# Performance work log

Hardware: AMD Instinct MI355X
Metric: run time of the kernel (lower is better)

Reference implementation:

```python
import jax, jax.numpy as jnp
import numpy as np

HIDDEN = 1024
NUM_HEADS = 16
HEAD_DIM = HIDDEN // NUM_HEADS


def setup_inputs() -> dict:
    key = jax.random.key(0)
    k1, k2, k3, k4, k5 = jax.random.split(key, 5)
    B, S, T, H = 2, 2048, 2048, HIDDEN
    scale = 0.02
    return {
        "query": jax.random.normal(k1, (B, S, H), dtype=jnp.float32),
        "key_value": jax.random.normal(k2, (B, T, H), dtype=jnp.float32),
        "Wq": jax.random.normal(k3, (H, H), dtype=jnp.float32) * scale,
        "Wkv": jax.random.normal(k4, (H, 2 * H), dtype=jnp.float32) * scale,
        "Wc": jax.random.normal(k5, (H, H), dtype=jnp.float32) * scale,
    }


def reference(query, key_value, Wq, Wkv, Wc):
    B, S, H = query.shape
    T = key_value.shape[1]
    nh, hd = NUM_HEADS, HEAD_DIM

    q = query @ Wq                                  # [B,S,H]
    kv = key_value @ Wkv                            # [B,T,2H]
    k, v = kv[..., :H], kv[..., H:]

    # [B, nh, S|T, hd]
    q = q.reshape(B, S, nh, hd).transpose(0, 2, 1, 3)
    k = k.reshape(B, T, nh, hd).transpose(0, 2, 1, 3)
    v = v.reshape(B, T, nh, hd).transpose(0, 2, 1, 3)

    scale = hd ** -0.5
    scores = jnp.einsum("bhsd,bhtd->bhst", q * scale, k)   # [B,nh,S,T]
    probs = jax.nn.softmax(scores, axis=-1)
    y = jnp.einsum("bhst,bhtd->bhsd", probs, v)             # [B,nh,S,hd]
    y = y.transpose(0, 2, 1, 3).reshape(B, S, H)
    return y @ Wc
```

## Files before the change

kernel.cpp:

```cpp
#include <hip/hip_runtime.h>
#include <hip/hip_bf16.h>


typedef unsigned short u16;
typedef __attribute__((ext_vector_type(4))) float float4v;
typedef __attribute__((ext_vector_type(4))) unsigned short u16x4;
typedef __attribute__((ext_vector_type(8))) short short8;
typedef __attribute__((ext_vector_type(4))) float floatx4;

__device__ __forceinline__ u16 f2bf(float f) {
  unsigned u = __float_as_uint(f);
  u += 0x7fffu + ((u >> 16) & 1u);
  return (u16)(u >> 16);
}

__device__ __forceinline__ float fast_exp2(float x) {
#if __has_builtin(__builtin_amdgcn_exp2f)
  return __builtin_amdgcn_exp2f(x);
#else
  return exp2f(x);
#endif
}

__device__ __forceinline__ unsigned pack_bf2(float a, float b) {
#if __has_builtin(__builtin_amdgcn_cvt_pk_bf16_f32)
  auto r = __builtin_amdgcn_cvt_pk_bf16_f32(a, b);
  unsigned u;
  __builtin_memcpy(&u, &r, 4);
  return u;
#else
  unsigned ua = __float_as_uint(a) + 0x7fffu + ((__float_as_uint(a) >> 16) & 1u);
  unsigned ub = __float_as_uint(b) + 0x7fffu + ((__float_as_uint(b) >> 16) & 1u);
  return __builtin_amdgcn_perm(ub, ua, 0x07060302u);
#endif
}

__device__ __forceinline__ void gld16(const void* g, void* l) {
  __builtin_amdgcn_global_load_lds(
      (const __attribute__((address_space(1))) void*)g,
      (__attribute__((address_space(3))) void*)l, 16, 0, 0);
}

__device__ __forceinline__ int swz4(int r) { return (r & 3) ^ ((r >> 2) & 3); }

__global__ void prep(const float* __restrict__ X, const float* __restrict__ KV,
                     const float* __restrict__ Wq, const float* __restrict__ Wkv,
                     const float* __restrict__ Wc,
                     u16* __restrict__ qin, u16* __restrict__ kvin,
                     u16* __restrict__ Wqt, u16* __restrict__ Wkvt,
                     u16* __restrict__ Wct) {
  __shared__ float tile[32][33];
  const int bid = blockIdx.x, t = threadIdx.x;
  if (bid < 8192) {
    const float* src = bid < 4096 ? X : KV;
    u16* dst = bid < 4096 ? qin : kvin;
    int i = (bid & 4095) * 256 + t;
    float4v v = ((const float4v*)src)[i];
    u16x4 o;
    o.x = f2bf(v.x); o.y = f2bf(v.y); o.z = f2bf(v.z); o.w = f2bf(v.w);
    ((u16x4*)dst)[i] = o;
  } else {
    int r = bid - 8192;
    const float* in;
    u16* out;
    int C, bx, by;
    if (r < 1024)      { in = Wq;  out = Wqt;  C = 1024; bx = r & 31; by = r >> 5; }
    else if (r < 3072) { r -= 1024; in = Wkv; out = Wkvt; C = 2048; bx = r & 63; by = r >> 6; }
    else               { r -= 3072; in = Wc;  out = Wct;  C = 1024; bx = r & 31; by = r >> 5; }
    const int tx = t & 31, ty = t >> 5;
#pragma unroll
    for (int i = 0; i < 32; i += 8)
      tile[ty + i][tx] = in[(size_t)(by * 32 + ty + i) * C + bx * 32 + tx];
    __syncthreads();
#pragma unroll
    for (int i = 0; i < 32; i += 8)
      out[(size_t)(bx * 32 + ty + i) * 1024 + by * 32 + tx] = f2bf(tile[tx][ty + i]);
  }
}

__global__ __launch_bounds__(256, 3) void gemm_qkv(const u16* __restrict__ qin,
                                                   const u16* __restrict__ kvin,
                                                   const u16* __restrict__ Wqt,
                                                   const u16* __restrict__ Wkvt,
                                                   u16* __restrict__ qp,
                                                   u16* __restrict__ kp,
                                                   u16* __restrict__ vt,
                                                   float qscale) {
  __shared__ __align__(16) u16 As[2 * 4096];
  __shared__ __align__(16) u16 Bs[2 * 4096];
  const int t = threadIdx.x;
  const int w = t >> 6, l = t & 63;
  const int lane15 = l & 15, quad = l >> 4;
  const int wm = w >> 1, wn = w & 1;
  const int bm = blockIdx.y * 128;

  const int bx = blockIdx.x;
  const int mode = bx >> 3;
  const u16* A = (mode == 0) ? qin : kvin;
  const u16* Bt = (mode == 0) ? Wqt : Wkvt;
  const int bn = (mode == 2) ? 1024 + (bx - 16) * 128 : (bx & 7) * 128;

  const int srow = t >> 2;
  const int scol = (((t & 3) ^ swz4(srow)) << 3);
  const u16* ag0 = A + (size_t)(bm + srow) * 1024 + scol;
  const u16* ag1 = ag0 + (size_t)64 * 1024;
  const u16* bg0 = Bt + (size_t)(bn + srow) * 1024 + scol;
  const u16* bg1 = bg0 + (size_t)64 * 1024;

  int afo[4], bfo[4];
#pragma unroll
  for (int mi = 0; mi < 4; ++mi) {
    int row = wm * 64 + mi * 16 + lane15;
    afo[mi] = row * 32 + ((quad ^ swz4(row)) << 3);
  }
#pragma unroll
  for (int ni = 0; ni < 4; ++ni) {
    int row = wn * 64 + ni * 16 + lane15;
    bfo[ni] = row * 32 + ((quad ^ swz4(row)) << 3);
  }

  floatx4 acc[4][4] = {};
  const bool vswap = (mode == 2);

  auto stage = [&](int kt, int buf) {
    gld16(ag0 + kt, &As[buf * 4096 + t * 8]);
    gld16(ag1 + kt, &As[buf * 4096 + 2048 + t * 8]);
    gld16(bg0 + kt, &Bs[buf * 4096 + t * 8]);
    gld16(bg1 + kt, &Bs[buf * 4096 + 2048 + t * 8]);
  };
  auto compute = [&](int buf) {
    short8 af[4], bf[4];
#pragma unroll
    for (int mi = 0; mi < 4; ++mi) af[mi] = *(const short8*)&As[buf * 4096 + afo[mi]];
#pragma unroll
    for (int ni = 0; ni < 4; ++ni) bf[ni] = *(const short8*)&Bs[buf * 4096 + bfo[ni]];
    if (!vswap) {
#pragma unroll
      for (int mi = 0; mi < 4; ++mi)
#pragma unroll
        for (int ni = 0; ni < 4; ++ni)
          acc[mi][ni] = __builtin_amdgcn_mfma_f32_16x16x32_bf16(af[mi], bf[ni],
                                                                acc[mi][ni], 0, 0, 0);
    } else {
#pragma unroll
      for (int mi = 0; mi < 4; ++mi)
#pragma unroll
        for (int ni = 0; ni < 4; ++ni)
          acc[mi][ni] = __builtin_amdgcn_mfma_f32_16x16x32_bf16(bf[ni], af[mi],
                                                                acc[mi][ni], 0, 0, 0);
    }
  };

  stage(0, 0);
  __syncthreads();
  for (int kt = 0; kt < 1024; kt += 64) {
    if (kt + 32 < 1024) stage(kt + 32, 1);
    compute(0);
    __syncthreads();
    if (kt + 64 < 1024) stage(kt + 64, 0);
    compute(1);
    __syncthreads();
  }

  if (mode == 0) {
#pragma unroll
    for (int mi = 0; mi < 4; ++mi)
#pragma unroll
      for (int ni = 0; ni < 4; ++ni) {
        int col = bn + wn * 64 + ni * 16 + lane15;
#pragma unroll
        for (int r = 0; r < 4; ++r) {
          int row = bm + wm * 64 + mi * 16 + quad * 4 + r;
          qp[(size_t)row * 1024 + col] = f2bf(acc[mi][ni][r] * qscale);
        }
      }
  } else if (mode == 1) {
#pragma unroll
    for (int mi = 0; mi < 4; ++mi)
#pragma unroll
      for (int ni = 0; ni < 4; ++ni) {
        int col = bn + wn * 64 + ni * 16 + lane15;
#pragma unroll
        for (int r = 0; r < 4; ++r) {
          int row = bm + wm * 64 + mi * 16 + quad * 4 + r;
          kp[(size_t)row * 1024 + col] = f2bf(acc[mi][ni][r]);
        }
      }
  } else {
    const int b = bm >> 11;
    const int tbase = (bm & 2047) + wm * 64;
#pragma unroll
    for (int mi = 0; mi < 4; ++mi)
#pragma unroll
      for (int ni = 0; ni < 4; ++ni) {
        int tloc = tbase + mi * 16 + lane15;
#pragma unroll
        for (int r = 0; r < 4; ++r) {
          int wc = (bn - 1024) + wn * 64 + ni * 16 + quad * 4 + r;
          vt[(size_t)(b * 1024 + wc) * 2048 + tloc] = f2bf(acc[mi][ni][r]);
        }
      }
  }
}

template <typename OutT, int NI>
__device__ __forceinline__ void gemm_body(const u16* __restrict__ A,
                                          const u16* __restrict__ Bt,
                                          OutT* __restrict__ C,
                                          int N, int lda, int Klen, float scale,
                                          int bm, int bn,
                                          u16* As, u16* Bs) {
  const int t = threadIdx.x;
  const int w = t >> 6, l = t & 63;
  const int lane15 = l & 15, quad = l >> 4;
  const int wm = w >> 1, wn = w & 1;
  const int BSZ = NI * 1024;

  const int srow = t >> 2;
  const int scol = (((t & 3) ^ swz4(srow)) << 3);
  const u16* ag0 = A + (size_t)(bm + srow) * lda + scol;
  const u16* ag1 = ag0 + (size_t)64 * lda;
  const u16* bg0 = Bt + (size_t)(bn + srow) * lda + scol;
  const u16* bg1 = bg0 + (size_t)64 * lda;

  int afo[4], bfo[NI];
#pragma unroll
  for (int mi = 0; mi < 4; ++mi) {
    int row = wm * 64 + mi * 16 + lane15;
    afo[mi] = row * 32 + ((quad ^ swz4(row)) << 3);
  }
#pragma unroll
  for (int ni = 0; ni < NI; ++ni) {
    int row = wn * (NI * 16) + ni * 16 + lane15;
    bfo[ni] = row * 32 + ((quad ^ swz4(row)) << 3);
  }

  floatx4 acc[4][NI] = {};

  auto stage = [&](int kt, int ab, int bb) {
    gld16(ag0 + kt, &As[ab + t * 8]);
    gld16(ag1 + kt, &As[ab + 2048 + t * 8]);
    gld16(bg0 + kt, &Bs[bb + t * 8]);
    if (NI == 4) gld16(bg1 + kt, &Bs[bb + 2048 + t * 8]);
  };
  auto compute = [&](int ab, int bb) {
    short8 af[4], bf[NI];
#pragma unroll
    for (int mi = 0; mi < 4; ++mi) af[mi] = *(const short8*)&As[ab + afo[mi]];
#pragma unroll
    for (int ni = 0; ni < NI; ++ni) bf[ni] = *(const short8*)&Bs[bb + bfo[ni]];
#pragma unroll
    for (int mi = 0; mi < 4; ++mi)
#pragma unroll
      for (int ni = 0; ni < NI; ++ni)
        acc[mi][ni] = __builtin_amdgcn_mfma_f32_16x16x32_bf16(af[mi], bf[ni],
                                                              acc[mi][ni], 0, 0, 0);
  };

  stage(0, 0, 0);
  __syncthreads();
  for (int kt = 0; kt < Klen; kt += 64) {
    if (kt + 32 < Klen) stage(kt + 32, 4096, BSZ);
    compute(0, 0);
    __syncthreads();
    if (kt + 64 < Klen) stage(kt + 64, 0, 0);
    compute(4096, BSZ);
    __syncthreads();
  }

#pragma unroll
  for (int mi = 0; mi < 4; ++mi)
#pragma unroll
    for (int ni = 0; ni < NI; ++ni) {
      int col = bn + wn * (NI * 16) + ni * 16 + lane15;
#pragma unroll
      for (int r = 0; r < 4; ++r) {
        int row = bm + wm * 64 + mi * 16 + quad * 4 + r;
        if constexpr (sizeof(OutT) == 4)
          C[(size_t)row * N + col] = acc[mi][ni][r] * scale;
        else
          C[(size_t)row * N + col] = f2bf(acc[mi][ni][r] * scale);
      }
    }
}

__global__ __launch_bounds__(256, 4) void gemm_out(const u16* __restrict__ A,
                                                   const u16* __restrict__ Bt,
                                                   float* __restrict__ C) {
  __shared__ __align__(16) u16 As[2 * 4096];
  __shared__ __align__(16) u16 Bs[2 * 2048];
  gemm_body<float, 2>(A, Bt, C, 1024, 1024, 1024, 1.0f, blockIdx.y * 128,
                      blockIdx.x * 64, As, Bs);
}

__global__ __launch_bounds__(512) void attn_kern(const u16* __restrict__ Q,
                                                 const u16* __restrict__ KP,
                                                 const u16* __restrict__ VT,
                                                 u16* __restrict__ Y) {
  __shared__ __align__(16) u16 Ks[2 * 4096];
  __shared__ __align__(16) u16 VTs[2 * 4096];
  __shared__ __align__(16) u16 Ps[8192];
  const int t = threadIdx.x, w = t >> 6, l = t & 63;
  const int lane15 = l & 15, quad = l >> 4;
  const int bh = blockIdx.y, b = bh >> 4, h = bh & 15;
  const int qrow0 = b * 2048 + blockIdx.x * 128;
  const int xm = lane15 & 7;

  short8 qf[2];
#pragma unroll
  for (int ks = 0; ks < 2; ++ks)
    qf[ks] = *(const short8*)&Q[(size_t)(qrow0 + w * 16 + lane15) * 1024 +
                                h * 64 + ks * 32 + quad * 8];

  const short8 vones = {0x3F80, 0x3F80, 0x3F80, 0x3F80,
                        0x3F80, 0x3F80, 0x3F80, 0x3F80};

  floatx4 yacc[4] = {};
  floatx4 lacc = {};

  const int srow = t >> 3;
  const int scol = (((t & 7) ^ (srow & 7)) << 3);
  const u16* kg = KP + (size_t)(b * 2048 + srow) * 1024 + h * 64 + scol;
  const u16* vg = VT + (size_t)(bh * 64 + srow) * 2048 + scol;

  const int prow = (w * 16 + lane15) * 64;
  int kfo[2][4], vfo[2][4], pwo[4], pro[2];
#pragma unroll
  for (int ks = 0; ks < 2; ++ks)
#pragma unroll
    for (int ti = 0; ti < 4; ++ti)
      kfo[ks][ti] = (ti * 16 + lane15) * 64 + (((ks * 4 + quad) ^ xm) << 3);
#pragma unroll
  for (int ts = 0; ts < 2; ++ts) {
#pragma unroll
    for (int ni = 0; ni < 4; ++ni)
      vfo[ts][ni] = (ni * 16 + lane15) * 64 + (((ts * 4 + quad) ^ xm) << 3);
    pro[ts] = prow + (((ts * 4 + quad) ^ xm) << 3);
  }
#pragma unroll
  for (int ti = 0; ti < 4; ++ti)
    pwo[ti] = prow + (((ti * 2 + (quad >> 1)) ^ xm) << 3) + ((quad & 1) << 2);

  auto stage = [&](int t0n, int buf) {
    gld16(kg + (size_t)t0n * 1024, &Ks[buf + t * 8]);
    gld16(vg + t0n, &VTs[buf + t * 8]);
  };
  auto compute = [&](int buf) {
    floatx4 sacc[4] = {};
#pragma unroll
    for (int ks = 0; ks < 2; ++ks)
#pragma unroll
      for (int ti = 0; ti < 4; ++ti) {
        short8 kf = *(const short8*)&Ks[buf + kfo[ks][ti]];
        sacc[ti] = __builtin_amdgcn_mfma_f32_16x16x32_bf16(kf, qf[ks], sacc[ti], 0, 0, 0);
      }
#pragma unroll
    for (int ti = 0; ti < 4; ++ti) {
      float p0 = fast_exp2(sacc[ti][0]);
      float p1 = fast_exp2(sacc[ti][1]);
      float p2 = fast_exp2(sacc[ti][2]);
      float p3 = fast_exp2(sacc[ti][3]);
      uint2 pk;
      pk.x = pack_bf2(p0, p1);
      pk.y = pack_bf2(p2, p3);
      *(uint2*)&Ps[pwo[ti]] = pk;
    }
#pragma unroll
    for (int ts = 0; ts < 2; ++ts) {
      short8 pf = *(const short8*)&Ps[pro[ts]];
      lacc = __builtin_amdgcn_mfma_f32_16x16x32_bf16(pf, vones, lacc, 0, 0, 0);
#pragma unroll
      for (int ni = 0; ni < 4; ++ni) {
        short8 vf = *(const short8*)&VTs[buf + vfo[ts][ni]];
        yacc[ni] = __builtin_amdgcn_mfma_f32_16x16x32_bf16(pf, vf, yacc[ni], 0, 0, 0);
      }
    }
  };

  stage(0, 0);
  __syncthreads();
  for (int t0 = 0; t0 < 2048; t0 += 128) {
    if (t0 + 64 < 2048) stage(t0 + 64, 4096);
    compute(0);
    __syncthreads();
    if (t0 + 128 < 2048) stage(t0 + 128, 0);
    compute(4096);
    __syncthreads();
  }

#pragma unroll
  for (int r = 0; r < 4; ++r) {
    float linv = 1.0f / lacc[r];
    int row = qrow0 + w * 16 + quad * 4 + r;
#pragma unroll
    for (int ni = 0; ni < 4; ++ni)
      Y[(size_t)row * 1024 + h * 64 + ni * 16 + lane15] = f2bf(yacc[ni][r] * linv);
  }
}

extern "C" void kernel_launch(void* const* d_in, const int* in_sizes, int n_in,
                              void* d_out, int out_size, void* d_ws, size_t ws_size,
                              hipStream_t stream) {
  const float* query = (const float*)d_in[0];
  const float* key_value = (const float*)d_in[1];
  const float* Wq = (const float*)d_in[2];
  const float* Wkv = (const float*)d_in[3];
  const float* Wc = (const float*)d_in[4];
  float* out = (float*)d_out;

  const size_t MB = 1024 * 1024;
  char* ws = (char*)d_ws;
  u16* qin  = (u16*)(ws + 0 * MB);
  u16* kvin = (u16*)(ws + 8 * MB);
  u16* Wqt  = (u16*)(ws + 16 * MB);
  u16* Wkvt = (u16*)(ws + 18 * MB);
  u16* Wct  = (u16*)(ws + 22 * MB);
  u16* qp   = (u16*)(ws + 24 * MB);
  u16* kp   = (u16*)(ws + 32 * MB);
  u16* vt   = (u16*)(ws + 40 * MB);
  u16* y    = (u16*)(ws + 48 * MB);

  prep<<<dim3(12288), dim3(256), 0, stream>>>(query, key_value, Wq, Wkv, Wc,
                                              qin, kvin, Wqt, Wkvt, Wct);
  const float qscale = 0.125f * 1.4426950408889634f;
  gemm_qkv<<<dim3(24, 32), dim3(256), 0, stream>>>(qin, kvin, Wqt, Wkvt,
                                                   qp, kp, vt, qscale);
  attn_kern<<<dim3(16, 32), dim3(512), 0, stream>>>(qp, kp, vt, y);
  gemm_out<<<dim3(16, 32), dim3(256), 0, stream>>>(y, Wct, out);
}
```

Before: 224.7 us.

## Stage GEMM epilogues through LDS and remap blocks for XCD locality

GEMM epilogues now write accumulators into swizzled shared memory and then emit 16-byte coalesced global stores, including the transposed V output that previously used scattered 2-byte stores. All three kernels switch to a 1D grid with a block-index remap that groups neighbouring tiles onto the same XCD to improve L2 reuse. This adds an extra LDS round trip and barriers in the epilogue.

```diff
diff --git a/kernel.cpp b/kernel.cpp
--- a/kernel.cpp
+++ b/kernel.cpp
@@ -86,15 +86,20 @@
                                                    u16* __restrict__ kp,
                                                    u16* __restrict__ vt,
                                                    float qscale) {
-  __shared__ __align__(16) u16 As[2 * 4096];
-  __shared__ __align__(16) u16 Bs[2 * 4096];
+  __shared__ __align__(16) u16 Shm[16384];
+  u16* As = Shm;
+  u16* Bs = Shm + 8192;
   const int t = threadIdx.x;
   const int w = t >> 6, l = t & 63;
   const int lane15 = l & 15, quad = l >> 4;
   const int wm = w >> 1, wn = w & 1;
-  const int bm = blockIdx.y * 128;
-
-  const int bx = blockIdx.x;
+
+  const int bid = blockIdx.x;
+  const int xr = bid & 7, g = bid >> 3;
+  const int bx = 12 * (xr & 1) + g % 12;
+  const int by = 8 * (xr >> 1) + g / 12;
+  const int bm = by * 128;
+
   const int mode = bx >> 3;
   const u16* A = (mode == 0) ? qin : kvin;
   const u16* Bt = (mode == 0) ? Wqt : Wkvt;
@@ -162,135 +167,129 @@
     __syncthreads();
   }
 
-  if (mode == 0) {
-#pragma unroll
-    for (int mi = 0; mi < 4; ++mi)
-#pragma unroll
-      for (int ni = 0; ni < 4; ++ni) {
-        int col = bn + wn * 64 + ni * 16 + lane15;
-#pragma unroll
-        for (int r = 0; r < 4; ++r) {
-          int row = bm + wm * 64 + mi * 16 + quad * 4 + r;
-          qp[(size_t)row * 1024 + col] = f2bf(acc[mi][ni][r] * qscale);
+  const float scale = (mode == 0) ? qscale : 1.0f;
+  __syncthreads();
+#pragma unroll
+  for (int mi = 0; mi < 4; ++mi)
+#pragma unroll
+    for (int ni = 0; ni < 4; ++ni)
+#pragma unroll
+      for (int r = 0; r < 4; ++r) {
+        int rl, cl;
+        if (!vswap) {
+          rl = wm * 64 + mi * 16 + quad * 4 + r;
+          cl = wn * 64 + ni * 16 + lane15;
+        } else {
+          rl = wn * 64 + ni * 16 + quad * 4 + r;
+          cl = wm * 64 + mi * 16 + lane15;
         }
+        Shm[rl * 128 + (cl ^ ((rl & 3) << 4))] = f2bf(acc[mi][ni][r] * scale);
       }
-  } else if (mode == 1) {
-#pragma unroll
-    for (int mi = 0; mi < 4; ++mi)
-#pragma unroll
-      for (int ni = 0; ni < 4; ++ni) {
-        int col = bn + wn * 64 + ni * 16 + lane15;
-#pragma unroll
-        for (int r = 0; r < 4; ++r) {
-          int row = bm + wm * 64 + mi * 16 + quad * 4 + r;
-          kp[(size_t)row * 1024 + col] = f2bf(acc[mi][ni][r]);
-        }
-      }
-  } else {
-    const int b = bm >> 11;
-    const int tbase = (bm & 2047) + wm * 64;
-#pragma unroll
-    for (int mi = 0; mi < 4; ++mi)
-#pragma unroll
-      for (int ni = 0; ni < 4; ++ni) {
-        int tloc = tbase + mi * 16 + lane15;
-#pragma unroll
-        for (int r = 0; r < 4; ++r) {
-          int wc = (bn - 1024) + wn * 64 + ni * 16 + quad * 4 + r;
-          vt[(size_t)(b * 1024 + wc) * 2048 + tloc] = f2bf(acc[mi][ni][r]);
-        }
-      }
-  }
-}
-
-template <typename OutT, int NI>
-__device__ __forceinline__ void gemm_body(const u16* __restrict__ A,
-                                          const u16* __restrict__ Bt,
-                                          OutT* __restrict__ C,
-                                          int N, int lda, int Klen, float scale,
-                                          int bm, int bn,
-                                          u16* As, u16* Bs) {
+  __syncthreads();
+#pragma unroll
+  for (int j = 0; j < 8; ++j) {
+    int c = t + j * 256;
+    int row = c >> 4, ch = c & 15;
+    short8 v = *(const short8*)&Shm[row * 128 + ((ch ^ ((row & 3) << 1)) << 3)];
+    if (mode == 0)
+      *(short8*)&qp[(size_t)(bm + row) * 1024 + bn + ch * 8] = v;
+    else if (mode == 1)
+      *(short8*)&kp[(size_t)(bm + row) * 1024 + bn + ch * 8] = v;
+    else {
+      int b = bm >> 11;
+      *(short8*)&vt[(size_t)(b * 1024 + (bn - 1024) + row) * 2048 +
+                    (bm & 2047) + ch * 8] = v;
+    }
+  }
+}
+
+__global__ __launch_bounds__(256, 4) void gemm_out(const u16* __restrict__ A,
+                                                   const u16* __restrict__ Bt,
+                                                   float* __restrict__ C) {
+  __shared__ __align__(16) u16 Shm[16384];
+  u16* As = Shm;
+  u16* Bs = Shm + 8192;
+  float* Shf = (float*)Shm;
   const int t = threadIdx.x;
   const int w = t >> 6, l = t & 63;
   const int lane15 = l & 15, quad = l >> 4;
   const int wm = w >> 1, wn = w & 1;
-  const int BSZ = NI * 1024;
+
+  const int bid = blockIdx.x;
+  const int xr = bid & 7, g = bid >> 3;
+  const int bx = 8 * (xr & 1) + g % 8;
+  const int by = 8 * (xr >> 1) + g / 8;
+  const int bm = by * 128, bn = bx * 64;
 
   const int srow = t >> 2;
   const int scol = (((t & 3) ^ swz4(srow)) << 3);
-  const u16* ag0 = A + (size_t)(bm + srow) * lda + scol;
-  const u16* ag1 = ag0 + (size_t)64 * lda;
-  const u16* bg0 = Bt + (size_t)(bn + srow) * lda + scol;
-  const u16* bg1 = bg0 + (size_t)64 * lda;
-
-  int afo[4], bfo[NI];
+  const u16* ag0 = A + (size_t)(bm + srow) * 1024 + scol;
+  const u16* ag1 = ag0 + (size_t)64 * 1024;
+  const u16* bg0 = Bt + (size_t)(bn + srow) * 1024 + scol;
+
+  int afo[4], bfo[2];
 #pragma unroll
   for (int mi = 0; mi < 4; ++mi) {
     int row = wm * 64 + mi * 16 + lane15;
     afo[mi] = row * 32 + ((quad ^ swz4(row)) << 3);
   }
 #pragma unroll
-  for (int ni = 0; ni < NI; ++ni) {
-    int row = wn * (NI * 16) + ni * 16 + lane15;
+  for (int ni = 0; ni < 2; ++ni) {
+    int row = wn * 32 + ni * 16 + lane15;
     bfo[ni] = row * 32 + ((quad ^ swz4(row)) << 3);
   }
 
-  floatx4 acc[4][NI] = {};
-
-  auto stage = [&](int kt, int ab, int bb) {
-    gld16(ag0 + kt, &As[ab + t * 8]);
-    gld16(ag1 + kt, &As[ab + 2048 + t * 8]);
-    gld16(bg0 + kt, &Bs[bb + t * 8]);
-    if (NI == 4) gld16(bg1 + kt, &Bs[bb + 2048 + t * 8]);
-  };
-  auto compute = [&](int ab, int bb) {
-    short8 af[4], bf[NI];
-#pragma unroll
-    for (int mi = 0; mi < 4; ++mi) af[mi] = *(const short8*)&As[ab + afo[mi]];
-#pragma unroll
-    for (int ni = 0; ni < NI; ++ni) bf[ni] = *(const short8*)&Bs[bb + bfo[ni]];
+  floatx4 acc[4][2] = {};
+
+  auto stage = [&](int kt, int buf) {
+    gld16(ag0 + kt, &As[buf * 4096 + t * 8]);
+    gld16(ag1 + kt, &As[buf * 4096 + 2048 + t * 8]);
+    gld16(bg0 + kt, &Bs[buf * 2048 + t * 8]);
+  };
+  auto compute = [&](int buf) {
+    short8 af[4], bf[2];
+#pragma unroll
+    for (int mi = 0; mi < 4; ++mi) af[mi] = *(const short8*)&As[buf * 4096 + afo[mi]];
+#pragma unroll
+    for (int ni = 0; ni < 2; ++ni) bf[ni] = *(const short8*)&Bs[buf * 2048 + bfo[ni]];
 #pragma unroll
     for (int mi = 0; mi < 4; ++mi)
 #pragma unroll
-      for (int ni = 0; ni < NI; ++ni)
+      for (int ni = 0; ni < 2; ++ni)
         acc[mi][ni] = __builtin_amdgcn_mfma_f32_16x16x32_bf16(af[mi], bf[ni],
                                                               acc[mi][ni], 0, 0, 0);
   };
 
-  stage(0, 0, 0);
-  __syncthreads();
-  for (int kt = 0; kt < Klen; kt += 64) {
-    if (kt + 32 < Klen) stage(kt + 32, 4096, BSZ);
-    compute(0, 0);
-    __syncthreads();
-    if (kt + 64 < Klen) stage(kt + 64, 0, 0);
-    compute(4096, BSZ);
-    __syncthreads();
-  }
-
+  stage(0, 0);
+  __syncthreads();
+  for (int kt = 0; kt < 1024; kt += 64) {
+    if (kt + 32 < 1024) stage(kt + 32, 1);
+    compute(0);
+    __syncthreads();
+    if (kt + 64 < 1024) stage(kt + 64, 0);
+    compute(1);
+    __syncthreads();
+  }
+
+  __syncthreads();
 #pragma unroll
   for (int mi = 0; mi < 4; ++mi)
 #pragma unroll
-    for (int ni = 0; ni < NI; ++ni) {
-      int col = bn + wn * (NI * 16) + ni * 16 + lane15;
+    for (int ni = 0; ni < 2; ++ni)
 #pragma unroll
       for (int r = 0; r < 4; ++r) {
-        int row = bm + wm * 64 + mi * 16 + quad * 4 + r;
-        if constexpr (sizeof(OutT) == 4)
-          C[(size_t)row * N + col] = acc[mi][ni][r] * scale;
-        else
-          C[(size_t)row * N + col] = f2bf(acc[mi][ni][r] * scale);
+        int rl = wm * 64 + mi * 16 + quad * 4 + r;
+        int cl = wn * 32 + ni * 16 + lane15;
+        Shf[rl * 64 + (cl ^ ((rl & 3) << 4))] = acc[mi][ni][r];
       }
-    }
-}
-
-__global__ __launch_bounds__(256, 4) void gemm_out(const u16* __restrict__ A,
-                                                   const u16* __restrict__ Bt,
-                                                   float* __restrict__ C) {
-  __shared__ __align__(16) u16 As[2 * 4096];
-  __shared__ __align__(16) u16 Bs[2 * 2048];
-  gemm_body<float, 2>(A, Bt, C, 1024, 1024, 1024, 1.0f, blockIdx.y * 128,
-                      blockIdx.x * 64, As, Bs);
+  __syncthreads();
+#pragma unroll
+  for (int j = 0; j < 8; ++j) {
+    int c = t + j * 256;
+    int row = c >> 4, ch = c & 15;
+    float4v v = *(const float4v*)&Shf[row * 64 + ((ch ^ ((row & 3) << 2)) << 2)];
+    *(float4v*)&C[(size_t)(bm + row) * 1024 + bn + ch * 4] = v;
+  }
 }
 
 __global__ __launch_bounds__(512) void attn_kern(const u16* __restrict__ Q,
@@ -302,8 +301,13 @@
   __shared__ __align__(16) u16 Ps[8192];
   const int t = threadIdx.x, w = t >> 6, l = t & 63;
   const int lane15 = l & 15, quad = l >> 4;
-  const int bh = blockIdx.y, b = bh >> 4, h = bh & 15;
-  const int qrow0 = b * 2048 + blockIdx.x * 128;
+
+  const int bid = blockIdx.x;
+  const int xr = bid & 7, g = bid >> 3;
+  const int bxt = 8 * (xr & 1) + g % 8;
+  const int bh = 8 * (xr >> 1) + g / 8;
+  const int b = bh >> 4, h = bh & 15;
+  const int qrow0 = b * 2048 + bxt * 128;
   const int xm = lane15 & 7;
 
   short8 qf[2];
@@ -423,8 +427,8 @@
   prep<<<dim3(12288), dim3(256), 0, stream>>>(query, key_value, Wq, Wkv, Wc,
                                               qin, kvin, Wqt, Wkvt, Wct);
   const float qscale = 0.125f * 1.4426950408889634f;
-  gemm_qkv<<<dim3(24, 32), dim3(256), 0, stream>>>(qin, kvin, Wqt, Wkvt,
-                                                   qp, kp, vt, qscale);
-  attn_kern<<<dim3(16, 32), dim3(512), 0, stream>>>(qp, kp, vt, y);
-  gemm_out<<<dim3(16, 32), dim3(256), 0, stream>>>(y, Wct, out);
-}
+  gemm_qkv<<<dim3(768), dim3(256), 0, stream>>>(qin, kvin, Wqt, Wkvt,
+                                                qp, kp, vt, qscale);
+  attn_kern<<<dim3(512), dim3(512), 0, stream>>>(qp, kp, vt, y);
+  gemm_out<<<dim3(512), dim3(256), 0, stream>>>(y, Wct, out);
+}
```

Measured after the change: 209.3 us. 6.8% less time.
